# Kernel tuning notes

Measured on AMD Instinct MI355X. Metric: run time of the kernel, lower is better.

Reference implementation:

```python
import jax, jax.numpy as jnp
import numpy as np

B, S, HID = 2, 2048, 4096
H, KV, D = 32, 8, 128          # heads, kv heads, head_dim
G = H // KV                    # num_key_value_groups
THETA = 10000.0
SCALE = 1.0 / np.sqrt(D)
NEG_INF = -1e9


def rotate_half(x):
    x1, x2 = x[..., : D // 2], x[..., D // 2 :]
    return jnp.concatenate([-x2, x1], axis=-1)


def rope_tables(seq_len):
    inv_freq = 1.0 / (THETA ** (jnp.arange(0, D, 2, dtype=jnp.float32) / D))
    t = jnp.arange(seq_len, dtype=jnp.float32)
    freqs = jnp.outer(t, inv_freq)              # [S, D/2]
    emb = jnp.concatenate([freqs, freqs], -1)   # [S, D]
    return jnp.cos(emb), jnp.sin(emb)


def setup_inputs() -> dict:
    key = jax.random.key(0)
    ks = jax.random.split(key, 5)
    w = 0.02
    x = jax.random.normal(ks[0], (B, S, HID), jnp.float32)
    Wq = jax.random.normal(ks[1], (HID, H * D), jnp.float32) * w
    Wk = jax.random.normal(ks[2], (HID, KV * D), jnp.float32) * w
    Wv = jax.random.normal(ks[3], (HID, KV * D), jnp.float32) * w
    Wo = jax.random.normal(ks[4], (H * D, HID), jnp.float32) * w
    position_ids = jnp.broadcast_to(jnp.arange(S, dtype=jnp.int32), (B, S))
    causal = jnp.where(
        jnp.arange(S)[:, None] >= jnp.arange(S)[None, :], 0.0, NEG_INF
    ).astype(jnp.float32)
    attention_mask = jnp.broadcast_to(causal, (B, 1, S, S))
    return {
        "by_pass_hidden_states": x,
        "attention_mask": attention_mask,
        "position_ids": position_ids,
        "Wq": Wq,
        "Wk": Wk,
        "Wv": Wv,
        "Wo": Wo,
    }


def reference(by_pass_hidden_states, attention_mask, position_ids, Wq, Wk, Wv, Wo):
    x = by_pass_hidden_states
    # QKV projections (weights stored [in, out])
    q = (x @ Wq).reshape(B, S, H, D).transpose(0, 2, 1, 3)    # [B,H,S,D]
    k = (x @ Wk).reshape(B, S, KV, D).transpose(0, 2, 1, 3)   # [B,KV,S,D]
    v = (x @ Wv).reshape(B, S, KV, D).transpose(0, 2, 1, 3)   # [B,KV,S,D]
    # RoPE
    cos_t, sin_t = rope_tables(S)
    cos = cos_t[position_ids][:, None]   # [B,1,S,D]
    sin = sin_t[position_ids][:, None]
    q = q * cos + rotate_half(q) * sin
    k = k * cos + rotate_half(k) * sin
    # GQA attention without materializing repeated K/V: group query heads
    qg = q.reshape(B, KV, G, S, D)
    scores = jnp.einsum("bkgsd,bktd->bkgst", qg, k) * SCALE   # [B,KV,G,S,S]
    scores = scores.reshape(B, H, S, S) + attention_mask
    probs = jax.nn.softmax(scores.astype(jnp.float32), axis=-1).astype(x.dtype)
    ctx = jnp.einsum("bkgst,bktd->bkgsd", probs.reshape(B, KV, G, S, S), v)
    ctx = ctx.reshape(B, H, S, D).transpose(0, 2, 1, 3).reshape(B, S, H * D)
    return ctx @ Wo
```

## Files before the change

kernel.cpp:

```cpp
#include <hip/hip_runtime.h>
#include <cstdint>
#include <cstddef>

#define B_   2
#define S_   2048
#define HID_ 4096
#define H_   32
#define KV_  8
#define D_   128
#define M_   (B_*S_)
#define QSTR 6144

typedef __attribute__((ext_vector_type(8))) short bf16x8;
typedef __attribute__((ext_vector_type(4))) float f32x4;
typedef __attribute__((ext_vector_type(16))) float f32x16;
typedef __attribute__((ext_vector_type(4))) unsigned int u32x4;
typedef unsigned short u16;
typedef unsigned int   u32;

#define KSC (0.08838834764831845f * 1.4426950408889634f)

__device__ __forceinline__ float bf2f(u16 v){ u32 u = ((u32)v) << 16; return __builtin_bit_cast(float, u); }
__device__ __forceinline__ u16 f2bf(float f){
  u32 u = __builtin_bit_cast(u32, f);
  u32 r = u + 0x7fffu + ((u >> 16) & 1u);
  return (u16)(r >> 16);
}

__device__ __forceinline__ void gload_lds16(const void* g, void* lds){
  __builtin_amdgcn_global_load_lds(
      (const __attribute__((address_space(1))) void*)g,
      (__attribute__((address_space(3))) void*)lds, 16, 0, 0);
}

#define BAR() __builtin_amdgcn_s_barrier()

__global__ void cast_f32_bf16(const float* __restrict__ in, u16* __restrict__ out, int n){
  int i = (blockIdx.x * blockDim.x + threadIdx.x) * 4;
  if (i >= n) return;
  float4 v = *(const float4*)(in + i);
  ushort4 o;
  o.x = f2bf(v.x); o.y = f2bf(v.y); o.z = f2bf(v.z); o.w = f2bf(v.w);
  *(ushort4*)(out + i) = o;
}

__global__ __launch_bounds__(256) void tcast_all(const float* __restrict__ Wq, const float* __restrict__ Wk,
                                                 const float* __restrict__ Wv, const float* __restrict__ Wo,
                                                 u16* __restrict__ WT, u16* __restrict__ WoT){
  int bid = blockIdx.x;
  const float* W; u16* Dp; int Nd, kx, ny;
  if (bid < 4096){       W = Wq; Dp = WT;                         Nd = 4096; kx = bid & 63;        ny = bid >> 6; }
  else if (bid < 5120){  W = Wk; Dp = WT + (size_t)4096 * 4096;   Nd = 1024; kx = (bid-4096) & 63; ny = (bid-4096) >> 6; }
  else if (bid < 6144){  W = Wv; Dp = WT + (size_t)5120 * 4096;   Nd = 1024; kx = (bid-5120) & 63; ny = (bid-5120) >> 6; }
  else {                 W = Wo; Dp = WoT;                        Nd = 4096; kx = (bid-6144) & 63; ny = (bid-6144) >> 6; }
  __shared__ __align__(16) u16 t[64][65];
  int k0 = kx * 64, n0 = ny * 64;
  int lx = threadIdx.x & 15, ly = threadIdx.x >> 4;
  #pragma unroll
  for (int rr = 0; rr < 4; ++rr){
    int r = rr * 16 + ly;
    float4 v = *(const float4*)(W + (size_t)(k0 + r) * Nd + n0 + lx * 4);
    t[lx*4+0][r] = f2bf(v.x);
    t[lx*4+1][r] = f2bf(v.y);
    t[lx*4+2][r] = f2bf(v.z);
    t[lx*4+3][r] = f2bf(v.w);
  }
  __syncthreads();
  #pragma unroll
  for (int rr = 0; rr < 4; ++rr){
    int r = rr * 16 + ly;
    ushort4 o;
    o.x = t[r][lx*4+0]; o.y = t[r][lx*4+1]; o.z = t[r][lx*4+2]; o.w = t[r][lx*4+3];
    *(ushort4*)(Dp + (size_t)(n0 + r) * 4096 + k0 + lx * 4) = o;
  }
}

__global__ __launch_bounds__(256) void vtrans(const u16* __restrict__ QKV, u16* __restrict__ Vt){
  __shared__ __align__(16) u16 t[64][65];
  int stile = blockIdx.x;
  int b = blockIdx.y >> 4, vt = blockIdx.y & 15;
  int s0 = stile * 64, c0 = vt * 64;
  int lx = threadIdx.x & 15, ly = threadIdx.x >> 4;
  #pragma unroll
  for (int rr = 0; rr < 4; ++rr){
    int r = rr * 16 + ly;
    ushort4 v = *(const ushort4*)(QKV + (size_t)(b*S_ + s0 + r) * QSTR + 5120 + c0 + lx*4);
    t[lx*4+0][r]=v.x; t[lx*4+1][r]=v.y; t[lx*4+2][r]=v.z; t[lx*4+3][r]=v.w;
  }
  __syncthreads();
  #pragma unroll
  for (int rr = 0; rr < 4; ++rr){
    int r = rr * 16 + ly;
    ushort4 o;
    o.x=t[r][lx*4+0]; o.y=t[r][lx*4+1]; o.z=t[r][lx*4+2]; o.w=t[r][lx*4+3];
    *(ushort4*)(Vt + (size_t)(b*1024 + c0 + r) * S_ + s0 + lx*4) = o;
  }
}

__global__ void rope_k(u16* __restrict__ X, const int* __restrict__ pos, int hshift, int stride){
  int idx = blockIdx.x * 256 + threadIdx.x;
  int i = idx & 63;
  int h = (idx >> 6) & ((1 << hshift) - 1);
  int t = idx >> (6 + hshift);
  u16* p0 = X + (size_t)t * stride + h * D_ + i;
  float x1 = bf2f(p0[0]), x2 = bf2f(p0[64]);
  float fpos = (float)pos[t];
  float invf = exp2f(-(float)(2 * i) * (13.287712379549449f / 128.0f));
  float f = fpos * invf;
  float sv = __sinf(f), cv = __cosf(f);
  p0[0]  = f2bf(x1 * cv - x2 * sv);
  p0[64] = f2bf(x2 * cv + x1 * sv);
}

#define STG_A(PB, HALF, KT) do{ \
  gload_lds16(Ag + off0 + (size_t)(HALF)*1048576 + (size_t)(KT)*128, \
              (char*)smem + (PB)*32768 + (HALF)*16384 + w*1024); \
  gload_lds16(Ag + off0 + 524288 + (size_t)(HALF)*1048576 + (size_t)(KT)*128, \
              (char*)smem + (PB)*32768 + (HALF)*16384 + 8192 + w*1024); }while(0)
#define STG_B(PB, HALF, KT) do{ \
  gload_lds16(Bg + off0 + (size_t)(HALF)*1048576 + (size_t)(KT)*128, \
              (char*)smem + 65536 + (PB)*32768 + (HALF)*16384 + w*1024); \
  gload_lds16(Bg + off0 + 524288 + (size_t)(HALF)*1048576 + (size_t)(KT)*128, \
              (char*)smem + 65536 + (PB)*32768 + (HALF)*16384 + 8192 + w*1024); }while(0)

#define RD_A(DST, PP, HALF) do{ \
  _Pragma("unroll") for (int ks = 0; ks < 2; ++ks) \
  _Pragma("unroll") for (int m = 0; m < 4; ++m) \
    DST[ks][m] = *(const bf16x8*)&smem[(PP)*16384 + (HALF)*8192 + aRowBase + m*1024 + csw[ks]]; }while(0)
#define RD_B(DST, PP, HALF) do{ \
  _Pragma("unroll") for (int ks = 0; ks < 2; ++ks) \
  _Pragma("unroll") for (int n = 0; n < 2; ++n) \
    DST[ks][n] = *(const bf16x8*)&smem[32768 + (PP)*16384 + (HALF)*8192 + bRowBase + n*1024 + csw[ks]]; }while(0)

template<int MO, int NO>
__device__ __forceinline__ void mfma_quad(f32x4 (&acc)[8][4],
                                          const bf16x8 (&af)[2][4], const bf16x8 (&bf)[2][2]){
  __builtin_amdgcn_s_setprio(1);
  #pragma unroll
  for (int ks = 0; ks < 2; ++ks)
    #pragma unroll
    for (int m = 0; m < 4; ++m)
      #pragma unroll
      for (int n = 0; n < 2; ++n)
        acc[MO+m][NO+n] = __builtin_amdgcn_mfma_f32_16x16x32_bf16(af[ks][m], bf[ks][n], acc[MO+m][NO+n], 0, 0, 0);
  __builtin_amdgcn_s_setprio(0);
}

template<bool OUTF32>
__global__ __launch_bounds__(512, 2) void gemm256(const u16* __restrict__ A, const u16* __restrict__ Bt,
                                                  void* __restrict__ C, int Nn, int mt){
  __shared__ __align__(16) u16 smem[65536];
  const int tid = threadIdx.x;
  const int l = tid & 63, w = tid >> 6;
  const int lr = l & 15, lk = l >> 4;
  const int wr = w >> 2, wc = w & 3;

  const int nwg = gridDim.x;
  const int sbid = ((int)blockIdx.x & 7) * (nwg >> 3) + ((int)blockIdx.x >> 3);
  const int bx = sbid % mt, by = sbid / mt;
  const size_t arow0 = (size_t)bx * 256;
  const size_t brow0 = (size_t)by * 256;
  const char* Ag = (const char*)(A + arow0 * 4096);
  const char* Bg = (const char*)(Bt + brow0 * 4096);

  const size_t off0 = (size_t)(w * 8 + (l >> 3)) * 8192 + (size_t)(((l & 7) ^ (l >> 3)) << 4);

  const int aRowBase = (wr*64 + lr) * 64;
  const int bRowBase = (wc*32 + lr) * 64;
  int csw[2];
  csw[0] = ((lk     ) ^ (lr & 7)) << 3;
  csw[1] = ((lk + 4) ^ (lr & 7)) << 3;

  f32x4 acc[8][4];
  #pragma unroll
  for (int i = 0; i < 8; ++i)
    #pragma unroll
    for (int j = 0; j < 4; ++j){ acc[i][j][0]=0.f; acc[i][j][1]=0.f; acc[i][j][2]=0.f; acc[i][j][3]=0.f; }

  STG_A(0, 0, 0); STG_B(0, 0, 0); STG_A(0, 1, 0); STG_B(0, 1, 0);
  STG_A(1, 0, 1); STG_B(1, 0, 1); STG_A(1, 1, 1); STG_B(1, 1, 1);
  asm volatile("s_waitcnt vmcnt(8)" ::: "memory");
  BAR();
  bf16x8 a0c[2][4], b0c[2][2], a1f[2][4], b1f[2][2];
  RD_A(a0c, 0, 0); RD_B(b0c, 0, 0);

  for (int t = 0; t < 64; ++t){
    const int P = t & 1;
    RD_A(a1f, P, 1);
    BAR();
    mfma_quad<0,0>(acc, a0c, b0c);
    BAR();
    if (t < 62){ STG_A(P, 0, t+2); STG_B(P, 0, t+2); }
    RD_B(b1f, P, 1);
    BAR();
    mfma_quad<4,0>(acc, a1f, b0c);
    BAR();
    if (t < 62){
      STG_A(P, 1, t+2);
      asm volatile("s_waitcnt vmcnt(6)" ::: "memory");
    } else if (t == 62){
      asm volatile("s_waitcnt vmcnt(0)" ::: "memory");
    }
    BAR();
    mfma_quad<4,2>(acc, a1f, b1f);
    BAR();
    if (t < 62){ STG_B(P, 1, t+2); }
    BAR();
    mfma_quad<0,2>(acc, a0c, b1f);
    if (t < 63){ RD_A(a0c, P^1, 0); RD_B(b0c, P^1, 0); }
    BAR();
  }

  #pragma unroll
  for (int mh = 0; mh < 2; ++mh)
    #pragma unroll
    for (int m = 0; m < 4; ++m)
      #pragma unroll
      for (int nh = 0; nh < 2; ++nh)
        #pragma unroll
        for (int n = 0; n < 2; ++n)
          #pragma unroll
          for (int j = 0; j < 4; ++j){
            size_t gr = arow0 + mh*128 + wr*64 + m*16 + lk*4 + j;
            size_t gc = brow0 + nh*128 + wc*32 + n*16 + lr;
            float v = acc[mh*4+m][nh*2+n][j];
            if (OUTF32) ((float*)C)[gr * Nn + gc] = v;
            else        ((u16*)C)[gr * Nn + gc] = f2bf(v);
          }
}

#define STG_B3(PB, KT) do{ \
  _Pragma("unroll") for (int r2 = 0; r2 < 3; ++r2) \
    gload_lds16(Bg + bsrc3[r2] + (size_t)(KT)*128, \
                (char*)smem + 65536 + (PB)*24576 + r2*8192 + w*1024); }while(0)

#define RD_B0(DST, PP) do{ \
  _Pragma("unroll") for (int ks = 0; ks < 2; ++ks) \
  _Pragma("unroll") for (int n = 0; n < 2; ++n) \
    DST[ks][n] = *(const bf16x8*)&smem[32768 + (PP)*12288 + bRowBase + n*1024 + csw[ks]]; }while(0)
#define RD_B1(DST, PP) do{ \
  _Pragma("unroll") for (int ks = 0; ks < 2; ++ks) \
    DST[ks] = *(const bf16x8*)&smem[32768 + (PP)*12288 + bRowBase + 2048 + csw[ks]]; }while(0)

__device__ __forceinline__ void mfma_pair16(f32x4 (&acc)[8][3], int MO,
                                            const bf16x8 (&af)[2][4], const bf16x8 (&bf)[2][2]){
  __builtin_amdgcn_s_setprio(1);
  #pragma unroll
  for (int ks = 0; ks < 2; ++ks)
    #pragma unroll
    for (int m = 0; m < 4; ++m)
      #pragma unroll
      for (int n = 0; n < 2; ++n)
        acc[MO+m][n] = __builtin_amdgcn_mfma_f32_16x16x32_bf16(af[ks][m], bf[ks][n], acc[MO+m][n], 0, 0, 0);
  __builtin_amdgcn_s_setprio(0);
}
__device__ __forceinline__ void mfma_pair8(f32x4 (&acc)[8][3], int MO,
                                           const bf16x8 (&af)[2][4], const bf16x8 (&bf)[2]){
  __builtin_amdgcn_s_setprio(1);
  #pragma unroll
  for (int ks = 0; ks < 2; ++ks)
    #pragma unroll
    for (int m = 0; m < 4; ++m)
      acc[MO+m][2] = __builtin_amdgcn_mfma_f32_16x16x32_bf16(af[ks][m], bf[ks], acc[MO+m][2], 0, 0, 0);
  __builtin_amdgcn_s_setprio(0);
}

__global__ __launch_bounds__(512, 2) void gemm192(const u16* __restrict__ A, const u16* __restrict__ Bt,
                                                  u16* __restrict__ C, int Nn, int mt){
  __shared__ __align__(16) u16 smem[57344];
  const int tid = threadIdx.x;
  const int l = tid & 63, w = tid >> 6;
  const int lr = l & 15, lk = l >> 4;
  const int wr = w >> 2, wc = w & 3;

  const int nwg = gridDim.x;
  const int sbid = ((int)blockIdx.x & 7) * (nwg >> 3) + ((int)blockIdx.x >> 3);
  const int bx = sbid % mt, by = sbid / mt;
  const size_t arow0 = (size_t)bx * 256;
  const size_t bcol0 = (size_t)by * 192;
  const char* Ag = (const char*)(A + arow0 * 4096);
  const char* Bg = (const char*)(Bt + bcol0 * 4096);

  const size_t off0 = (size_t)(w * 8 + (l >> 3)) * 8192 + (size_t)(((l & 7) ^ (l >> 3)) << 4);
  size_t bsrc3[3];
  #pragma unroll
  for (int r2 = 0; r2 < 3; ++r2){
    int idx = r2 * 512 + tid;
    int row = idx >> 3, ch = idx & 7;
    bsrc3[r2] = (size_t)row * 8192 + (size_t)((ch ^ (row & 7)) << 4);
  }

  const int aRowBase = (wr*64 + lr) * 64;
  const int bRowBase = (wc*48 + lr) * 64;
  int csw[2];
  csw[0] = ((lk     ) ^ (lr & 7)) << 3;
  csw[1] = ((lk + 4) ^ (lr & 7)) << 3;

  f32x4 acc[8][3];
  #pragma unroll
  for (int i = 0; i < 8; ++i)
    #pragma unroll
    for (int j = 0; j < 3; ++j){ acc[i][j][0]=0.f; acc[i][j][1]=0.f; acc[i][j][2]=0.f; acc[i][j][3]=0.f; }

  STG_A(0, 0, 0); STG_A(0, 1, 0); STG_B3(0, 0);
  STG_A(1, 0, 1); STG_A(1, 1, 1); STG_B3(1, 1);
  asm volatile("s_waitcnt vmcnt(7)" ::: "memory");
  BAR();
  bf16x8 a0c[2][4], a1f[2][4], b0c[2][2], b1f[2];
  RD_A(a0c, 0, 0); RD_B0(b0c, 0);

  for (int t = 0; t < 64; ++t){
    const int P = t & 1;
    RD_A(a1f, P, 1);
    BAR();
    mfma_pair16(acc, 0, a0c, b0c);
    BAR();
    if (t < 62){ STG_A(P, 0, t+2); }
    RD_B1(b1f, P);
    BAR();
    mfma_pair16(acc, 4, a1f, b0c);
    BAR();
    if (t < 62){
      STG_A(P, 1, t+2);
      asm volatile("s_waitcnt vmcnt(4)" ::: "memory");
    } else if (t == 62){
      asm volatile("s_waitcnt vmcnt(0)" ::: "memory");
    }
    BAR();
    mfma_pair8(acc, 4, a1f, b1f);
    BAR();
    if (t < 62){ STG_B3(P, t+2); }
    BAR();
    mfma_pair8(acc, 0, a0c, b1f);
    if (t < 63){ RD_A(a0c, P^1, 0); RD_B0(b0c, P^1); }
    BAR();
  }

  #pragma unroll
  for (int mh = 0; mh < 2; ++mh)
    #pragma unroll
    for (int m = 0; m < 4; ++m)
      #pragma unroll
      for (int f = 0; f < 3; ++f)
        #pragma unroll
        for (int j = 0; j < 4; ++j){
          size_t gr = arow0 + mh*128 + wr*64 + m*16 + lk*4 + j;
          size_t gc = bcol0 + wc*48 + f*16 + lr;
          C[gr * Nn + gc] = f2bf(acc[mh*4+m][f][j]);
        }
}

__global__ __launch_bounds__(512, 2) void attn_k(const u16* __restrict__ QKV,
                                                 const u16* __restrict__ Vtg,
                                                 const int* __restrict__ pos,
                                                 u16* __restrict__ ctx){
  __shared__ __align__(16) u16 smem[32768];
  const int tid = threadIdx.x;
  const int l = tid & 63, w = tid >> 6;
  const int lane31 = l & 31, hi = l >> 5;
  const int hb = blockIdx.x;
  const int b = hb >> 5, h = hb & 31, kvh = h >> 2;
  const int y = blockIdx.y;
  const int qb = (y < 4) ? (7 - y) : (y - 4);
  const int q0w = qb * 256 + w * 32;
  const int qg = q0w + lane31;

  const u16* Qp = QKV + (size_t)b * S_ * QSTR + (size_t)h * D_;
  const char* Kp = (const char*)(QKV + (size_t)b * S_ * QSTR + 4096 + (size_t)kvh * D_);
  const char* Vp = (const char*)(Vtg + ((size_t)b * 1024 + kvh * 128) * S_);

  bf16x8 qf[8];
  #pragma unroll
  for (int dt = 0; dt < 8; ++dt)
    qf[dt] = *(const bf16x8*)(Qp + (size_t)qg * QSTR + dt * 16 + hi * 8);

  {
    float fp = (float)pos[b * S_ + qg];
    #pragma unroll
    for (int dt = 0; dt < 4; ++dt){
      bf16x8 lo = qf[dt], hi8 = qf[dt + 4], nlo, nhi;
      #pragma unroll
      for (int j = 0; j < 8; ++j){
        int d = dt * 16 + hi * 8 + j;
        float invf = exp2f(-(float)(2 * d) * (13.287712379549449f / 128.0f));
        float f = fp * invf;
        float sv = __sinf(f), cv = __cosf(f);
        float x1 = bf2f((u16)lo[j]), x2 = bf2f((u16)hi8[j]);
        nlo[j] = (short)f2bf(x1 * cv - x2 * sv);
        nhi[j] = (short)f2bf(x2 * cv + x1 * sv);
      }
      qf[dt] = nlo; qf[dt + 4] = nhi;
    }
  }

  const int krow0 = (2*w)*4 + (l >> 4), krow1 = krow0 + 4;
  const size_t koff0 = (size_t)krow0 * (QSTR*2) + (((l & 15) << 4) ^ ((krow0 & 7) << 4));
  const size_t koff1 = (size_t)krow1 * (QSTR*2) + (((l & 15) << 4) ^ ((krow1 & 7) << 4));
  const int vrow0 = (2*w)*8 + (l >> 3), vrow1 = vrow0 + 8;
  const size_t voff0 = (size_t)vrow0 * (S_*2) + (((l & 7) << 4) ^ ((vrow0 & 7) << 4));
  const size_t voff1 = (size_t)vrow1 * (S_*2) + (((l & 7) << 4) ^ ((vrow1 & 7) << 4));

  f32x16 acc[4];
  #pragma unroll
  for (int dt = 0; dt < 4; ++dt)
    #pragma unroll
    for (int i = 0; i < 16; ++i) acc[dt][i] = 0.f;
  float mrow = -3e38f, lsum = 0.f;

  const int nt = qb * 4 + 4;

  auto STAGE = [&](int t, int bufn){
    char* Kb = (char*)smem + bufn * 16384;
    char* Vb = (char*)smem + 32768 + bufn * 16384;
    size_t kb = (size_t)t * 64 * (QSTR*2);
    size_t vb = (size_t)t * 128;
    gload_lds16(Kp + kb + koff0, Kb + (2*w)*1024);
    gload_lds16(Kp + kb + koff1, Kb + (2*w+1)*1024);
    gload_lds16(Vp + vb + voff0, Vb + (2*w)*1024);
    gload_lds16(Vp + vb + voff1, Vb + (2*w+1)*1024);
  };

  STAGE(0, 0);
  __syncthreads();
  int buf = 0;
  for (int t = 0; t < nt; ++t){
    if (t + 1 < nt) STAGE(t + 1, buf ^ 1);
    const int kbase = t * 64;
    if (kbase <= q0w + 31){
      const char* Kb = (const char*)smem + buf * 16384;
      const char* Vb = (const char*)smem + 32768 + buf * 16384;
      const int swz = (lane31 & 7) << 4;

      f32x16 s0, s1;
      #pragma unroll
      for (int i = 0; i < 16; ++i){ s0[i] = 0.f; s1[i] = 0.f; }
      __builtin_amdgcn_s_setprio(1);
      #pragma unroll
      for (int dt = 0; dt < 8; ++dt){
        bf16x8 kf = *(const bf16x8*)(Kb + lane31*256 + ((dt*32 + hi*16) ^ swz));
        s0 = __builtin_amdgcn_mfma_f32_32x32x16_bf16(kf, qf[dt], s0, 0, 0, 0);
      }
      #pragma unroll
      for (int dt = 0; dt < 8; ++dt){
        bf16x8 kf = *(const bf16x8*)(Kb + (32 + lane31)*256 + ((dt*32 + hi*16) ^ swz));
        s1 = __builtin_amdgcn_mfma_f32_32x32x16_bf16(kf, qf[dt], s1, 0, 0, 0);
      }
      __builtin_amdgcn_s_setprio(0);

      if (kbase + 63 > q0w){
        int thr = qg - kbase;
        #pragma unroll
        for (int r = 0; r < 16; ++r){
          int kc = (r & 3) + 8*(r >> 2) + 4*hi;
          s0[r] = (kc > thr)      ? -1e30f : s0[r];
          s1[r] = (kc + 32 > thr) ? -1e30f : s1[r];
        }
      }

      float tmax = s0[0];
      #pragma unroll
      for (int r = 1; r < 16; ++r) tmax = fmaxf(tmax, s0[r]);
      #pragma unroll
      for (int r = 0; r < 16; ++r) tmax = fmaxf(tmax, s1[r]);
      tmax = fmaxf(tmax, __shfl_xor(tmax, 32));
      if (!__all(tmax - mrow <= 62.7f)){
        float mn = fmaxf(mrow, tmax);
        float rf = exp2f((mrow - mn) * KSC);
        mrow = mn;
        lsum *= rf;
        #pragma unroll
        for (int dt = 0; dt < 4; ++dt)
          #pragma unroll
          for (int i = 0; i < 16; ++i) acc[dt][i] *= rf;
      }
      float ps = 0.f;
      #pragma unroll
      for (int r = 0; r < 16; ++r){
        float a = exp2f((s0[r] - mrow) * KSC);
        float c = exp2f((s1[r] - mrow) * KSC);
        s0[r] = a; s1[r] = c; ps += a + c;
      }
      ps += __shfl_xor(ps, 32);
      lsum += ps;

      u32 pw[16];
      #pragma unroll
      for (int g = 0; g < 4; ++g){
        pw[2*g]     = (u32)f2bf(s0[4*g])   | ((u32)f2bf(s0[4*g+1]) << 16);
        pw[2*g+1]   = (u32)f2bf(s0[4*g+2]) | ((u32)f2bf(s0[4*g+3]) << 16);
        pw[8+2*g]   = (u32)f2bf(s1[4*g])   | ((u32)f2bf(s1[4*g+1]) << 16);
        pw[8+2*g+1] = (u32)f2bf(s1[4*g+2]) | ((u32)f2bf(s1[4*g+3]) << 16);
      }

      #pragma unroll
      for (int kt = 0; kt < 4; ++kt){
        u32 W0 = pw[kt*4+0], W1 = pw[kt*4+1], W2 = pw[kt*4+2], W3 = pw[kt*4+3];
        u32 x0 = hi ? W0 : W2;
        u32 x1 = hi ? W1 : W3;
        u32 y0 = __shfl_xor(x0, 32);
        u32 y1 = __shfl_xor(x1, 32);
        u32 w0 = hi ? y0 : W0;
        u32 w1 = hi ? y1 : W1;
        u32 w2 = hi ? W2 : y0;
        u32 w3 = hi ? W3 : y1;
        u32x4 pk; pk[0]=w0; pk[1]=w1; pk[2]=w2; pk[3]=w3;
        bf16x8 pa = __builtin_bit_cast(bf16x8, pk);
        __builtin_amdgcn_s_setprio(1);
        #pragma unroll
        for (int dt = 0; dt < 4; ++dt){
          bf16x8 vf = *(const bf16x8*)(Vb + (dt*32 + lane31)*128 + ((kt*32 + hi*16) ^ swz));
          acc[dt] = __builtin_amdgcn_mfma_f32_32x32x16_bf16(vf, pa, acc[dt], 0, 0, 0);
        }
        __builtin_amdgcn_s_setprio(0);
      }
    }
    __syncthreads();
    buf ^= 1;
  }

  __syncthreads();
  u16* Ot = smem + w * 4096;
  float inv = 1.f / lsum;
  #pragma unroll
  for (int dt = 0; dt < 4; ++dt)
    #pragma unroll
    for (int r = 0; r < 16; ++r){
      int d = dt*32 + (r & 3) + 8*(r >> 2) + 4*hi;
      Ot[lane31*128 + (d ^ ((lane31 & 15) << 2))] = f2bf(acc[dt][r] * inv);
    }
  u16* outp = ctx + ((size_t)(b * S_ + q0w)) * HID_ + h * D_;
  #pragma unroll
  for (int it = 0; it < 16; ++it){
    int id = it * 64 + l;
    int q = id >> 5;
    int c4 = (id & 31) * 4;
    ushort4 vv = *(const ushort4*)(Ot + q*128 + (c4 ^ ((q & 15) << 2)));
    *(ushort4*)(outp + (size_t)q * HID_ + c4) = vv;
  }
}

extern "C" void kernel_launch(void* const* d_in, const int* in_sizes, int n_in,
                              void* d_out, int out_size, void* d_ws, size_t ws_size,
                              hipStream_t stream) {
  const float* x  = (const float*)d_in[0];
  const int*   pos = (const int*)d_in[2];
  const float* Wq = (const float*)d_in[3];
  const float* Wk = (const float*)d_in[4];
  const float* Wv = (const float*)d_in[5];
  const float* Wo = (const float*)d_in[6];

  char* ws = (char*)d_ws;
  u16* xb   = (u16*)(ws);
  u16* WT   = (u16*)(ws + ((size_t)32 << 20));
  u16* WoT  = (u16*)(ws + ((size_t)80 << 20));
  u16* QKVb = (u16*)(ws + ((size_t)112 << 20));
  u16* Vtg  = (u16*)(ws + ((size_t)32 << 20));

  cast_f32_bf16<<<16384, 256, 0, stream>>>(x, xb, HID_ * M_);
  tcast_all<<<10240, 256, 0, stream>>>(Wq, Wk, Wv, Wo, WT, WoT);
  gemm192<<<512, 512, 0, stream>>>(xb, WT, QKVb, 6144, 16);
  rope_k<<<8192, 256, 0, stream>>>(QKVb + 4096, pos, 3, QSTR);
  vtrans<<<dim3(32, 32), 256, 0, stream>>>(QKVb, Vtg);
  attn_k<<<dim3(64, 8), 512, 0, stream>>>(QKVb, Vtg, pos, xb);
  gemm256<true><<<256, 512, 0, stream>>>(xb, WoT, d_out, 4096, 16);
}
```

Before: 515.6 us.

## Fuse RoPE and V transpose kernels, grid-stride cast, skip fully masked score half

Merges the K RoPE kernel and the V transpose kernel into one launch that splits work by block index, which removes one kernel launch. The input cast becomes a grid-stride loop with far fewer blocks. In attention, the second 32-key score MFMA block is skipped when it lies entirely above the causal diagonal for this wave. That block was already masked to -1e30, so skipping it saves MFMA work, but it relies on the mask still setting those values even though s1 stays zero.

```diff
diff --git a/kernel.cpp b/kernel.cpp
--- a/kernel.cpp
+++ b/kernel.cpp
@@ -36,12 +36,13 @@
 #define BAR() __builtin_amdgcn_s_barrier()
 
 __global__ void cast_f32_bf16(const float* __restrict__ in, u16* __restrict__ out, int n){
-  int i = (blockIdx.x * blockDim.x + threadIdx.x) * 4;
-  if (i >= n) return;
-  float4 v = *(const float4*)(in + i);
-  ushort4 o;
-  o.x = f2bf(v.x); o.y = f2bf(v.y); o.z = f2bf(v.z); o.w = f2bf(v.w);
-  *(ushort4*)(out + i) = o;
+  int stride = gridDim.x * blockDim.x * 4;
+  for (int i = (blockIdx.x * blockDim.x + threadIdx.x) * 4; i < n; i += stride){
+    float4 v = *(const float4*)(in + i);
+    ushort4 o;
+    o.x = f2bf(v.x); o.y = f2bf(v.y); o.z = f2bf(v.z); o.w = f2bf(v.w);
+    *(ushort4*)(out + i) = o;
+  }
 }
 
 __global__ __launch_bounds__(256) void tcast_all(const float* __restrict__ Wq, const float* __restrict__ Wk,
@@ -75,41 +76,44 @@
   }
 }
 
-__global__ __launch_bounds__(256) void vtrans(const u16* __restrict__ QKV, u16* __restrict__ Vt){
-  __shared__ __align__(16) u16 t[64][65];
-  int stile = blockIdx.x;
-  int b = blockIdx.y >> 4, vt = blockIdx.y & 15;
-  int s0 = stile * 64, c0 = vt * 64;
-  int lx = threadIdx.x & 15, ly = threadIdx.x >> 4;
-  #pragma unroll
-  for (int rr = 0; rr < 4; ++rr){
-    int r = rr * 16 + ly;
-    ushort4 v = *(const ushort4*)(QKV + (size_t)(b*S_ + s0 + r) * QSTR + 5120 + c0 + lx*4);
-    t[lx*4+0][r]=v.x; t[lx*4+1][r]=v.y; t[lx*4+2][r]=v.z; t[lx*4+3][r]=v.w;
-  }
-  __syncthreads();
-  #pragma unroll
-  for (int rr = 0; rr < 4; ++rr){
-    int r = rr * 16 + ly;
-    ushort4 o;
-    o.x=t[r][lx*4+0]; o.y=t[r][lx*4+1]; o.z=t[r][lx*4+2]; o.w=t[r][lx*4+3];
-    *(ushort4*)(Vt + (size_t)(b*1024 + c0 + r) * S_ + s0 + lx*4) = o;
-  }
-}
-
-__global__ void rope_k(u16* __restrict__ X, const int* __restrict__ pos, int hshift, int stride){
-  int idx = blockIdx.x * 256 + threadIdx.x;
-  int i = idx & 63;
-  int h = (idx >> 6) & ((1 << hshift) - 1);
-  int t = idx >> (6 + hshift);
-  u16* p0 = X + (size_t)t * stride + h * D_ + i;
-  float x1 = bf2f(p0[0]), x2 = bf2f(p0[64]);
-  float fpos = (float)pos[t];
-  float invf = exp2f(-(float)(2 * i) * (13.287712379549449f / 128.0f));
-  float f = fpos * invf;
-  float sv = __sinf(f), cv = __cosf(f);
-  p0[0]  = f2bf(x1 * cv - x2 * sv);
-  p0[64] = f2bf(x2 * cv + x1 * sv);
+__global__ __launch_bounds__(256) void rope_vtrans(u16* __restrict__ QKV, u16* __restrict__ Vt,
+                                                   const int* __restrict__ pos){
+  int bid = blockIdx.x;
+  if (bid < 1024){
+    __shared__ __align__(16) u16 t[64][65];
+    int stile = bid & 31;
+    int rest = bid >> 5;
+    int b = rest >> 4, vt = rest & 15;
+    int s0 = stile * 64, c0 = vt * 64;
+    int lx = threadIdx.x & 15, ly = threadIdx.x >> 4;
+    #pragma unroll
+    for (int rr = 0; rr < 4; ++rr){
+      int r = rr * 16 + ly;
+      ushort4 v = *(const ushort4*)(QKV + (size_t)(b*S_ + s0 + r) * QSTR + 5120 + c0 + lx*4);
+      t[lx*4+0][r]=v.x; t[lx*4+1][r]=v.y; t[lx*4+2][r]=v.z; t[lx*4+3][r]=v.w;
+    }
+    __syncthreads();
+    #pragma unroll
+    for (int rr = 0; rr < 4; ++rr){
+      int r = rr * 16 + ly;
+      ushort4 o;
+      o.x=t[r][lx*4+0]; o.y=t[r][lx*4+1]; o.z=t[r][lx*4+2]; o.w=t[r][lx*4+3];
+      *(ushort4*)(Vt + (size_t)(b*1024 + c0 + r) * S_ + s0 + lx*4) = o;
+    }
+  } else {
+    int idx = (bid - 1024) * 256 + threadIdx.x;
+    int i = idx & 63;
+    int h = (idx >> 6) & 7;
+    int t = idx >> 9;
+    u16* p0 = QKV + 4096 + (size_t)t * QSTR + h * D_ + i;
+    float x1 = bf2f(p0[0]), x2 = bf2f(p0[64]);
+    float fpos = (float)pos[t];
+    float invf = exp2f(-(float)(2 * i) * (13.287712379549449f / 128.0f));
+    float f = fpos * invf;
+    float sv = __sinf(f), cv = __cosf(f);
+    p0[0]  = f2bf(x1 * cv - x2 * sv);
+    p0[64] = f2bf(x2 * cv + x1 * sv);
+  }
 }
 
 #define STG_A(PB, HALF, KT) do{ \
@@ -434,16 +438,19 @@
       f32x16 s0, s1;
       #pragma unroll
       for (int i = 0; i < 16; ++i){ s0[i] = 0.f; s1[i] = 0.f; }
+      const bool doS1 = (kbase + 32 <= q0w + 31);
       __builtin_amdgcn_s_setprio(1);
       #pragma unroll
       for (int dt = 0; dt < 8; ++dt){
         bf16x8 kf = *(const bf16x8*)(Kb + lane31*256 + ((dt*32 + hi*16) ^ swz));
         s0 = __builtin_amdgcn_mfma_f32_32x32x16_bf16(kf, qf[dt], s0, 0, 0, 0);
       }
-      #pragma unroll
-      for (int dt = 0; dt < 8; ++dt){
-        bf16x8 kf = *(const bf16x8*)(Kb + (32 + lane31)*256 + ((dt*32 + hi*16) ^ swz));
-        s1 = __builtin_amdgcn_mfma_f32_32x32x16_bf16(kf, qf[dt], s1, 0, 0, 0);
+      if (doS1){
+        #pragma unroll
+        for (int dt = 0; dt < 8; ++dt){
+          bf16x8 kf = *(const bf16x8*)(Kb + (32 + lane31)*256 + ((dt*32 + hi*16) ^ swz));
+          s1 = __builtin_amdgcn_mfma_f32_32x32x16_bf16(kf, qf[dt], s1, 0, 0, 0);
+        }
       }
       __builtin_amdgcn_s_setprio(0);
 
@@ -556,11 +563,10 @@
   u16* QKVb = (u16*)(ws + ((size_t)112 << 20));
   u16* Vtg  = (u16*)(ws + ((size_t)32 << 20));
 
-  cast_f32_bf16<<<16384, 256, 0, stream>>>(x, xb, HID_ * M_);
+  cast_f32_bf16<<<2048, 256, 0, stream>>>(x, xb, HID_ * M_);
   tcast_all<<<10240, 256, 0, stream>>>(Wq, Wk, Wv, Wo, WT, WoT);
   gemm192<<<512, 512, 0, stream>>>(xb, WT, QKVb, 6144, 16);
-  rope_k<<<8192, 256, 0, stream>>>(QKVb + 4096, pos, 3, QSTR);
-  vtrans<<<dim3(32, 32), 256, 0, stream>>>(QKVb, Vtg);
+  rope_vtrans<<<9216, 256, 0, stream>>>(QKVb, Vtg, pos);
   attn_k<<<dim3(64, 8), 512, 0, stream>>>(QKVb, Vtg, pos, xb);
   gemm256<true><<<256, 512, 0, stream>>>(xb, WoT, d_out, 4096, 16);
 }
```

Result: no change. 513.9 us (-0.3%).
